# Performance work log

Measured on AMD Instinct MI355X. Metric: run time of the kernel, lower is better.

## Reference

```python
import jax, jax.numpy as jnp
import numpy as np

N_FLUID, N_BOX, K_MAX, KS, NCELL = 6000, 3000, 80, 4, 64
RADIUS = np.float32(0.5 * 1.5 * 6 * 0.025)  # filter_extent / 2 = 0.1125


def _ball_to_cube(p):
    """Volume-preserving ball->cube mapping (open3d ContinuousConv convention).
    p: [..., 3] coordinates in the unit ball; returns coords in [-1,1]^3."""
    eps = 1e-12
    x, y, z = p[..., 0], p[..., 1], p[..., 2]
    sq = x * x + y * y + z * z
    norm = jnp.sqrt(sq)
    rxy2 = x * x + y * y
    # sphere -> cylinder (volume preserving)
    polar = 1.25 * z * z > rxy2
    s_pol = jnp.sqrt(3.0 * norm / (norm + jnp.abs(z) + eps))
    s_eq = norm / jnp.sqrt(rxy2 + eps)
    xc = jnp.where(polar, s_pol * x, s_eq * x)
    yc = jnp.where(polar, s_pol * y, s_eq * y)
    zc = jnp.where(polar, jnp.sign(z) * norm, 1.5 * z * s_eq)
    zero = sq < 1e-12
    xc = jnp.where(zero, 0.0, xc)
    yc = jnp.where(zero, 0.0, yc)
    zc = jnp.where(zero, 0.0, zc)
    # cylinder -> cube (area-preserving disc -> square on xy)
    rxy = jnp.sqrt(xc * xc + yc * yc)
    FP = 4.0 / np.pi
    safe_x = jnp.where(jnp.abs(xc) < eps, eps, xc)
    safe_y = jnp.where(jnp.abs(yc) < eps, eps, yc)
    cond = jnp.abs(xc) >= jnp.abs(yc)
    u1 = jnp.sign(xc) * rxy
    v1 = u1 * FP * jnp.arctan(yc / safe_x)
    v2 = jnp.sign(yc) * rxy
    u2 = v2 * FP * jnp.arctan(xc / safe_y)
    u = jnp.where(cond, u1, u2)
    v = jnp.where(cond, v1, v2)
    small = rxy < eps
    u = jnp.where(small, 0.0, u)
    v = jnp.where(small, 0.0, v)
    return jnp.stack([u, v, zc], axis=-1)


def build_neighbors(pos_in, pos_out, ignore_self):
    """Fixed-radius neighbor search (capped at K_MAX) + window + trilinear
    interpolation cells/weights. Returns idx [No,K], cells [No,K,8] int32,
    coef [No,K,8] (trilinear weight * poly6 window * validity)."""
    d = pos_in[None, :, :] - pos_out[:, None, :]            # [No,Ni,3]
    d2 = jnp.sum(d * d, axis=-1)
    if ignore_self:
        ii = jnp.arange(pos_out.shape[0])
        d2 = jnp.where(ii[:, None] == ii[None, :], jnp.inf, d2)
    neg = jnp.where(d2 <= RADIUS * RADIUS, -d2, -jnp.inf)
    vals, idx = jax.lax.top_k(neg, K_MAX)                   # [No,K]
    valid = (vals > -jnp.inf).astype(pos_in.dtype)
    rel = (pos_in[idx] - pos_out[:, None, :]) / RADIUS      # [No,K,3] unit ball
    r2 = jnp.sum(rel * rel, axis=-1)
    win = jnp.clip((1.0 - r2) ** 3, 0.0, 1.0) * valid       # poly6 window
    g = jnp.clip((_ball_to_cube(rel) + 1.0) * 0.5 * (KS - 1), 0.0, KS - 1.0)
    i0 = jnp.clip(jnp.floor(g), 0, KS - 2).astype(jnp.int32)
    t = g - i0.astype(g.dtype)
    cells, tw = [], []
    for dx in (0, 1):
        for dy in (0, 1):
            for dz in (0, 1):
                w = ((t[..., 0] if dx else 1.0 - t[..., 0])
                     * (t[..., 1] if dy else 1.0 - t[..., 1])
                     * (t[..., 2] if dz else 1.0 - t[..., 2]))
                cell = ((i0[..., 2] + dz) * KS + (i0[..., 1] + dy)) * KS + (i0[..., 0] + dx)
                cells.append(cell)
                tw.append(w)
    cells = jnp.stack(cells, axis=-1)                       # [No,K,8]
    coef = jnp.stack(tw, axis=-1) * win[..., None]          # [No,K,8]
    return idx, cells, coef


def apply_cconv(feats_in, idx, cells, coef, W, b):
    """Continuous conv: scatter neighbor feats into 64 kernel cells per query,
    then contract with the filter. W: [64, F, O]."""
    N, K = idx.shape
    F = feats_in.shape[-1]
    nf = feats_in[idx]                                      # [N,K,F]
    S = jnp.zeros((N * NCELL, F), feats_in.dtype)
    row = (jnp.arange(N, dtype=jnp.int32) * NCELL)[:, None]
    for c in range(8):                                      # 8 trilinear corners
        flat = (row + cells[..., c]).reshape(-1)
        S = S.at[flat].add((coef[..., c:c + 1] * nf).reshape(-1, F))
    return jnp.einsum('ncf,cfo->no', S.reshape(N, NCELL, F), W) + b


def setup_inputs() -> dict:
    key = jax.random.key(0)
    ks = jax.random.split(key, 16)

    def p(i, shape, scale=0.05):
        return (scale * jax.random.normal(ks[i], shape)).astype(jnp.float32)

    return {
        'pos': jax.random.uniform(ks[0], (N_FLUID, 3), dtype=jnp.float32),
        'vel': jax.random.normal(ks[1], (N_FLUID, 3), dtype=jnp.float32),
        'box': jax.random.uniform(ks[2], (N_BOX, 3), dtype=jnp.float32),
        'box_feats': jax.random.normal(ks[3], (N_BOX, 3), dtype=jnp.float32),
        'cf_w': p(4, (NCELL, 4, 32)), 'cf_b': jnp.zeros((32,), jnp.float32),
        'co_w': p(5, (NCELL, 3, 32)), 'co_b': jnp.zeros((32,), jnp.float32),
        'd0_w': p(6, (4, 32)), 'd0_b': jnp.zeros((32,), jnp.float32),
        'c1_w': p(7, (NCELL, 96, 64)), 'c1_b': jnp.zeros((64,), jnp.float32),
        'd1_w': p(8, (96, 64)), 'd1_b': jnp.zeros((64,), jnp.float32),
        'c2_w': p(9, (NCELL, 64, 64)), 'c2_b': jnp.zeros((64,), jnp.float32),
        'd2_w': p(10, (64, 64)), 'd2_b': jnp.zeros((64,), jnp.float32),
        'c3_w': p(11, (NCELL, 64, 3)), 'c3_b': jnp.zeros((3,), jnp.float32),
        'd3_w': p(12, (64, 3)), 'd3_b': jnp.zeros((3,), jnp.float32),
    }


def reference(pos, vel, box, box_feats, cf_w, cf_b, co_w, co_b, d0_w, d0_b,
              c1_w, c1_b, d1_w, d1_b, c2_w, c2_b, d2_w, d2_b, c3_w, c3_b,
              d3_w, d3_b):
    fidx, fcells, fcoef = build_neighbors(pos, pos, True)
    oidx, ocells, ocoef = build_neighbors(box, pos, False)
    ff = jnp.concatenate([jnp.ones_like(pos[:, :1]), vel], axis=-1)  # [N,4]
    a_cf = apply_cconv(ff, fidx, fcells, fcoef, cf_w, cf_b)
    a_co = apply_cconv(box_feats, oidx, ocells, ocoef, co_w, co_b)
    a_d0 = ff @ d0_w + d0_b
    x = jnp.concatenate([a_co, a_cf, a_d0], axis=-1)                 # [N,96]
    for cw, cb, dw, db in ((c1_w, c1_b, d1_w, d1_b),
                           (c2_w, c2_b, d2_w, d2_b),
                           (c3_w, c3_b, d3_w, d3_b)):
        h = jax.nn.relu(x)
        y = apply_cconv(h, fidx, fcells, fcoef, cw, cb) + (h @ dw + db)
        x = y + x if y.shape[-1] == x.shape[-1] else y
    return x * (1.0 / 128.0)  # pos_correction [N,3]
```

## Files before the change

### kernel.cpp

```cpp
#include <hip/hip_runtime.h>
#include <math.h>

namespace {

constexpr int NQ  = 6000;
constexpr int NB  = 3000;
constexpr int K   = 80;
constexpr float RAD = 0.1125f;
constexpr float R2  = RAD * RAD;
constexpr float EPSF = 1e-12f;

constexpr int GS  = 8;
constexpr int NC  = GS*GS*GS;
constexpr int NO  = 65 * 64;
constexpr int NBLK = (NQ + 3) / 4;
constexpr int NBLK8 = ((NBLK + 7) / 8) * 8;

typedef __attribute__((ext_vector_type(8))) short bf16x8;
typedef __attribute__((ext_vector_type(4))) float f32x4;

__device__ __forceinline__ float sgn(float x) {
    return (x > 0.f) ? 1.f : ((x < 0.f) ? -1.f : 0.f);
}

__device__ __forceinline__ unsigned int bf16rne(float f) {
    unsigned int u = __float_as_uint(f);
    return (u + 0x7fffu + ((u >> 16) & 1u)) >> 16;
}
__device__ __forceinline__ float bf16f(unsigned short u) {
    return __uint_as_float(((unsigned int)u) << 16);
}
__device__ __forceinline__ int cell_of(float x, float y, float z) {
    int cx = min(max((int)(x * (float)GS), 0), GS-1);
    int cy = min(max((int)(y * (float)GS), 0), GS-1);
    int cz = min(max((int)(z * (float)GS), 0), GS-1);
    return (cz*GS + cy)*GS + cx;
}

__device__ void coef_store(float ddx, float ddy, float ddz, int slot,
                           int* __restrict__ cells, float* __restrict__ coefs)
{
    float rx = ddx / RAD, ry = ddy / RAD, rz = ddz / RAD;
    float r2 = rx*rx + ry*ry + rz*rz;
    float w1 = 1.f - r2;
    float win = (w1 > 0.f) ? w1*w1*w1 : 0.f;
    float norm = sqrtf(r2);
    float rxy2 = rx*rx + ry*ry;
    float xc, yc, zc;
    if (r2 < 1e-12f) {
        xc = yc = zc = 0.f;
    } else if (1.25f * rz * rz > rxy2) {
        float s = sqrtf(3.0f * norm / (norm + fabsf(rz) + EPSF));
        xc = s * rx; yc = s * ry; zc = sgn(rz) * norm;
    } else {
        float s = norm / sqrtf(rxy2 + EPSF);
        xc = s * rx; yc = s * ry; zc = 1.5f * rz * s;
    }
    float rxy = sqrtf(xc*xc + yc*yc);
    const float FP = (float)(4.0 / M_PI);
    float u, v;
    if (rxy < EPSF) {
        u = 0.f; v = 0.f;
    } else if (fabsf(xc) >= fabsf(yc)) {
        float sx = (fabsf(xc) < EPSF) ? EPSF : xc;
        u = sgn(xc) * rxy;
        v = u * FP * atanf(yc / sx);
    } else {
        float sy = (fabsf(yc) < EPSF) ? EPSF : yc;
        v = sgn(yc) * rxy;
        u = v * FP * atanf(xc / sy);
    }
    float gx = fminf(fmaxf((u  + 1.f) * 0.5f * 3.f, 0.f), 3.f);
    float gy = fminf(fmaxf((v  + 1.f) * 0.5f * 3.f, 0.f), 3.f);
    float gz = fminf(fmaxf((zc + 1.f) * 0.5f * 3.f, 0.f), 3.f);
    int ix = min((int)floorf(gx), 2);
    int iy = min((int)floorf(gy), 2);
    int iz = min((int)floorf(gz), 2);
    float tx = gx - (float)ix, ty = gy - (float)iy, tz = gz - (float)iz;
    cells[slot] = iz*16 + iy*4 + ix;
    float wx[2] = {1.f - tx, tx}, wy[2] = {1.f - ty, ty}, wz[2] = {1.f - tz, tz};
    float* cf = coefs + (size_t)slot * 8;
#pragma unroll
    for (int c = 0; c < 8; ++c)
        cf[c] = wx[c >> 2] * wy[(c >> 1) & 1] * wz[c & 1] * win;
}

__global__ __launch_bounds__(512) void scan_kernel(
    const int* __restrict__ gcnt,
    int* __restrict__ gs_f, int* __restrict__ gs_b,
    int* __restrict__ cur_f, int* __restrict__ cur_b)
{
    __shared__ int tmp[NC];
    int tid = threadIdx.x;
#pragma unroll
    for (int a = 0; a < 2; ++a) {
        int cntv = gcnt[a*NC + tid];
        tmp[tid] = cntv;
        __syncthreads();
        for (int off = 1; off < NC; off <<= 1) {
            int v = (tid >= off) ? tmp[tid - off] : 0;
            __syncthreads();
            tmp[tid] += v;
            __syncthreads();
        }
        int* gsd = a ? gs_b : gs_f;
        int* cur = a ? cur_b : cur_f;
        int excl = tmp[tid] - cntv;
        gsd[tid] = excl;
        cur[tid] = excl;
        if (tid == NC - 1) gsd[NC] = tmp[tid];
        __syncthreads();
    }
}

__global__ __launch_bounds__(256) void scatter_pts_kernel(
    const float* __restrict__ pos, const float* __restrict__ box,
    int* __restrict__ cur_f, int* __restrict__ cur_b,
    float* __restrict__ spf, int* __restrict__ sif,
    float* __restrict__ spb, int* __restrict__ sib)
{
    int t = blockIdx.x * blockDim.x + threadIdx.x;
    if (t < NQ) {
        float x = pos[t*3], y = pos[t*3+1], z = pos[t*3+2];
        int dst = atomicAdd(&cur_f[cell_of(x,y,z)], 1);
        spf[dst*3] = x; spf[dst*3+1] = y; spf[dst*3+2] = z;
        sif[dst] = t;
    } else if (t < NQ + NB) {
        int b = t - NQ;
        float x = box[b*3], y = box[b*3+1], z = box[b*3+2];
        int dst = atomicAdd(&cur_b[cell_of(x,y,z)], 1);
        spb[dst*3] = x; spb[dst*3+1] = y; spb[dst*3+2] = z;
        sib[dst] = b;
    }
}

__global__ __launch_bounds__(256) void nn2gc_kernel(
    const float* __restrict__ pos,
    const float* __restrict__ spf, const int* __restrict__ sif, const int* __restrict__ gsf,
    const float* __restrict__ spb, const int* __restrict__ sib, const int* __restrict__ gsb,
    int* __restrict__ f_cnt, int* __restrict__ f_idx, float* __restrict__ f_d2,
    int* __restrict__ f_cell, float* __restrict__ f_coef,
    int* __restrict__ b_cnt, int* __restrict__ b_idx, float* __restrict__ b_d2,
    int* __restrict__ b_cell, float* __restrict__ b_coef)
{
    int gw = (blockIdx.x * blockDim.x + threadIdx.x) >> 6;
    int lane = threadIdx.x & 63;
    if (gw >= 2 * NQ) return;
    bool isF = gw < NQ;
    int wid = isF ? gw : gw - NQ;
    const float* sp = isF ? spf : spb;
    const int*   si = isF ? sif : sib;
    const int*   gs = isF ? gsf : gsb;
    int*   cnt   = isF ? f_cnt  : b_cnt;
    int*   idxs  = isF ? f_idx  : b_idx;
    float* d2s   = isF ? f_d2   : b_d2;
    int*   cells = isF ? f_cell : b_cell;
    float* coefs = isF ? f_coef : b_coef;
    float qx = pos[wid*3+0], qy = pos[wid*3+1], qz = pos[wid*3+2];
    int cx = min(max((int)(qx * (float)GS), 0), GS-1);
    int cy = min(max((int)(qy * (float)GS), 0), GS-1);
    int cz = min(max((int)(qz * (float)GS), 0), GS-1);
    int x0 = max(cx-1, 0), x1 = min(cx+1, GS-1);
    int base = wid * K;
    int c = 0;
    for (int dz = -1; dz <= 1; ++dz) {
        int z = cz + dz; if ((unsigned)z >= (unsigned)GS) continue;
        for (int dy = -1; dy <= 1; ++dy) {
            int y = cy + dy; if ((unsigned)y >= (unsigned)GS) continue;
            int row = (z*GS + y)*GS;
            int s0 = gs[row + x0], s1 = gs[row + x1 + 1];
            for (int j0 = s0; j0 < s1; j0 += 64) {
                int ii = j0 + lane;
                float d2 = 1e30f; int oj = 0;
                float ddx = 0.f, ddy = 0.f, ddz = 0.f;
                if (ii < s1) {
                    oj = si[ii];
                    ddx = sp[ii*3+0]-qx; ddy = sp[ii*3+1]-qy; ddz = sp[ii*3+2]-qz;
                    d2 = ddx*ddx + ddy*ddy + ddz*ddz;
                    if (isF && oj == wid) d2 = 1e30f;
                }
                bool hit = d2 <= R2;
                unsigned long long m = __ballot(hit);
                int pc = __popcll(m);
                if (pc == 0) continue;
                if (c + pc <= K) {
                    if (hit) {
                        int p = c + __popcll(m & ((1ull << lane) - 1ull));
                        idxs[base + p] = oj;
                        d2s [base + p] = d2;
                        coef_store(ddx, ddy, ddz, base + p, cells, coefs);
                    }
                    c += pc;
                } else {
                    while (m) {
                        int l = __ffsll((unsigned long long)m) - 1;
                        m &= m - 1ull;
                        float dd = __shfl(d2, l);
                        int jv = __shfl(oj, l);
                        float ax = __shfl(ddx, l), ay = __shfl(ddy, l), az = __shfl(ddz, l);
                        int slot = -1;
                        if (c < K) { slot = c; c++; }
                        else {
                            float mx = -1.f; int am = 0;
                            for (int s = 0; s < K; ++s) {
                                float v = d2s[base + s];
                                if (v > mx) { mx = v; am = s; }
                            }
                            if (dd < mx) slot = am;
                        }
                        if (slot >= 0 && lane == 0) {
                            idxs[base + slot] = jv;
                            d2s [base + slot] = dd;
                            coef_store(ax, ay, az, base + slot, cells, coefs);
                        }
                    }
                }
            }
        }
    }
    if (lane == 0) cnt[wid] = c;
}

template<int F>
__device__ void scatter_small_dev(
    const float* __restrict__ feats,
    const int* __restrict__ cnt, const int* __restrict__ nidx,
    const int* __restrict__ ncell, const float* __restrict__ ncoef,
    float* __restrict__ Sg, int blk)
{
    __shared__ __align__(16) float S4[4][64 * F];
    int tid = threadIdx.x, lane = tid & 63, w = tid >> 6;
    int n = blk * 4 + w;
    if (n >= NQ) return;
    float* Sw = S4[w];
    for (int i = lane; i < 64 * F; i += 64) Sw[i] = 0.f;
    int cn = cnt[n];
    int kk2 = 64 + lane;
    int cb1 = (lane < cn) ? ncell[n*K + lane] : 0;
    int j1  = (lane < cn) ? nidx [n*K + lane] : 0;
    int cb2 = (kk2 < cn) ? ncell[n*K + kk2] : 0;
    int j2  = (kk2 < cn) ? nidx [n*K + kk2] : 0;
    int c = lane & 7, f = lane >> 3;
    bool fok = f < F;
    const float* coefG = ncoef + (size_t)n * K * 8;

    float wgt = 0.f, v = 0.f; int cb = 0;
    if (cn > 0) {
        int j = __shfl(j1, 0); cb = __shfl(cb1, 0);
        if (fok) { wgt = coefG[c]; v = feats[(size_t)j * F + f]; }
    }
    for (int kk = 0; kk < cn; ++kk) {
        float wn = 0.f, vn = 0.f; int cbn = 0;
        int k1n = kk + 1;
        if (k1n < cn) {
            int jn = (k1n < 64) ? __shfl(j1, k1n) : __shfl(j2, k1n - 64);
            cbn    = (k1n < 64) ? __shfl(cb1, k1n) : __shfl(cb2, k1n - 64);
            if (fok) { wn = coefG[k1n*8 + c]; vn = feats[(size_t)jn * F + f]; }
        }
        if (fok) {
            int cell = cb + (c & 1)*16 + ((c >> 1) & 1)*4 + (c >> 2);
            Sw[cell*F + f] += wgt * v;
        }
        wgt = wn; v = vn; cb = cbn;
    }
    float* row = Sg + (size_t)n * (64 * F);
    for (int i = lane; i < 16 * F; i += 64)
        ((float4*)row)[i] = ((const float4*)Sw)[i];
}

__global__ __launch_bounds__(256) void scatter0_kernel(
    const float* __restrict__ ff,
    const int* __restrict__ f_cnt, const int* __restrict__ f_idx,
    const int* __restrict__ f_cell, const float* __restrict__ f_coef,
    const float* __restrict__ bfeat,
    const int* __restrict__ b_cnt, const int* __restrict__ b_idx,
    const int* __restrict__ b_cell, const float* __restrict__ b_coef,
    float* __restrict__ S_cf, float* __restrict__ S_co)
{
    constexpr int FB = (NQ + 3) / 4;
    if (blockIdx.x < FB)
        scatter_small_dev<4>(ff, f_cnt, f_idx, f_cell, f_coef, S_cf, blockIdx.x);
    else
        scatter_small_dev<3>(bfeat, b_cnt, b_idx, b_cell, b_coef, S_co, blockIdx.x - FB);
}

__global__ __launch_bounds__(256) void gemm0_kernel(
    const float* __restrict__ S_co, const float* __restrict__ S_cf,
    const float* __restrict__ coW, const float* __restrict__ cfW,
    const float* __restrict__ cob, const float* __restrict__ cfb,
    float* __restrict__ x1, int M)
{
    constexpr int O = 32, TX = 8, MT = 128, ASTR = 132;
    __shared__ float As[16][ASTR];
    __shared__ float Bs[16 * O];
    int which = blockIdx.y;
    const float* A    = which ? S_cf : S_co;
    const float* B    = which ? cfW  : coW;
    const float* bias = which ? cfb  : cob;
    int Kdim = which ? 256 : 192;
    int ooff = which ? 32 : 0;
    int tid = threadIdx.x;
    int tx = tid % TX, ty = tid / TX;
    int m0 = blockIdx.x * MT;
    int ntiles = Kdim >> 4;
    float acc[4][4] = {};
    for (int t = 0; t < ntiles; ++t) {
        int k0 = t << 4;
        __syncthreads();
#pragma unroll
        for (int l = 0; l < 2; ++l) {
            int idx = tid + l * 256;
            int mm = idx >> 2, k4 = idx & 3;
            int gm = m0 + mm; if (gm >= M) gm = M - 1;
            float4 av = *reinterpret_cast<const float4*>(A + (size_t)gm * Kdim + k0 + k4 * 4);
            As[k4*4+0][mm] = av.x; As[k4*4+1][mm] = av.y;
            As[k4*4+2][mm] = av.z; As[k4*4+3][mm] = av.w;
        }
        if (tid < 128)
            *reinterpret_cast<float4*>(&Bs[tid*4]) =
                *reinterpret_cast<const float4*>(B + (size_t)k0 * O + tid * 4);
        __syncthreads();
#pragma unroll
        for (int kk = 0; kk < 16; ++kk) {
            float4 av = *reinterpret_cast<const float4*>(&As[kk][ty*4]);
            float4 bv = *reinterpret_cast<const float4*>(&Bs[kk*O + tx*4]);
            float aa[4] = {av.x, av.y, av.z, av.w};
            float bb[4] = {bv.x, bv.y, bv.z, bv.w};
#pragma unroll
            for (int i = 0; i < 4; ++i)
#pragma unroll
                for (int jj = 0; jj < 4; ++jj)
                    acc[i][jj] += aa[i] * bb[jj];
        }
    }
#pragma unroll
    for (int i = 0; i < 4; ++i) {
        int gm = m0 + ty*4 + i;
        if (gm < M)
#pragma unroll
            for (int jj = 0; jj < 4; ++jj)
                x1[(size_t)gm * 96 + ooff + tx*4 + jj] = acc[i][jj] + bias[tx*4 + jj];
    }
}

template<int F>
__global__ __launch_bounds__(256) void gemmGm_kernel(
    const float* __restrict__ feats,
    const unsigned short* __restrict__ Bt,
    unsigned short* __restrict__ G,
    int M)
{
    constexpr int AST = F + 8;
    __shared__ unsigned short As[64 * AST];
    __shared__ unsigned short Bs[64 * AST];
    int tid = threadIdx.x, lane = tid & 63, wv = tid >> 6;
    int m0 = blockIdx.x * 64, no0 = blockIdx.y * 64;
    for (int i = tid; i < 64 * F / 4; i += 256) {
        int m = i / (F / 4), k4 = i % (F / 4);
        int gm = m0 + m; if (gm >= M) gm = M - 1;
        float4 av = *reinterpret_cast<const float4*>(feats + (size_t)gm * F + k4 * 4);
        uint2 o;
        o.x = bf16rne(fmaxf(av.x, 0.f)) | (bf16rne(fmaxf(av.y, 0.f)) << 16);
        o.y = bf16rne(fmaxf(av.z, 0.f)) | (bf16rne(fmaxf(av.w, 0.f)) << 16);
        *reinterpret_cast<uint2*>(As + m * AST + k4 * 4) = o;
    }
    for (int i = tid; i < 64 * F / 8; i += 256) {
        int n = i / (F / 8), k8 = i % (F / 8);
        *reinterpret_cast<uint4*>(Bs + n * AST + k8 * 8) =
            *reinterpret_cast<const uint4*>(Bt + (size_t)(no0 + n) * F + k8 * 8);
    }
    __syncthreads();
    int mr = lane & 15, quad = lane >> 4;
    f32x4 acc[4] = {{0.f,0.f,0.f,0.f},{0.f,0.f,0.f,0.f},
                    {0.f,0.f,0.f,0.f},{0.f,0.f,0.f,0.f}};
#pragma unroll
    for (int kc = 0; kc < F; kc += 32) {
        bf16x8 a = *reinterpret_cast<const bf16x8*>(As + (wv*16 + mr) * AST + kc + quad*8);
#pragma unroll
        for (int t = 0; t < 4; ++t) {
            bf16x8 b = *reinterpret_cast<const bf16x8*>(Bs + (t*16 + mr) * AST + kc + quad*8);
            acc[t] = __builtin_amdgcn_mfma_f32_16x16x32_bf16(a, b, acc[t], 0, 0, 0);
        }
    }
#pragma unroll
    for (int t = 0; t < 4; ++t) {
#pragma unroll
        for (int r = 0; r < 4; ++r) {
            int gm = m0 + wv*16 + quad*4 + r;
            if (gm < M)
                G[(size_t)gm * NO + no0 + t*16 + mr] = (unsigned short)bf16rne(acc[t][r]);
        }
    }
}

template<int FUSEY>
__global__ __launch_bounds__(256) void gatherG_kernel(
    const int* __restrict__ order,
    const int* __restrict__ cnt, const int* __restrict__ nidx,
    const int* __restrict__ ncell, const float* __restrict__ ncoef,
    const unsigned short* __restrict__ G,
    const float* __restrict__ cb, const float* __restrict__ db,
    const float* __restrict__ resid, float* __restrict__ out,
    const float* __restrict__ W3p, float* __restrict__ Y)
{
    __shared__ __align__(16) float coefL[4][K * 8];
    __shared__ float xs[4][64];
    __shared__ int qn[4];
    int lb = (blockIdx.x & 7) * (gridDim.x >> 3) + (blockIdx.x >> 3);
    int tid = threadIdx.x;
    int wv = tid >> 6, lane = tid & 63;
    int w = lb * 4 + wv;
    bool valid = w < NQ;
    if (!FUSEY && !valid) return;
    int n = valid ? order[w] : 0;
    int cn = valid ? cnt[n] : 0;
    {
        const float4* src = (const float4*)(ncoef + (size_t)n * K * 8);
        float4* dst = (float4*)coefL[wv];
        for (int i = lane; i < cn * 2; i += 64) dst[i] = src[i];
    }
    int kk2 = 64 + lane;
    int cb1 = (lane < cn) ? ncell[n*K + lane] : 0;
    int j1  = (lane < cn) ? nidx [n*K + lane] : 0;
    int cb2 = (kk2 < cn) ? ncell[n*K + kk2] : 0;
    int j2  = (kk2 < cn) ? nidx [n*K + kk2] : 0;
    float a0 = 0.f, a1 = 0.f, a2 = 0.f, a3 = 0.f;
    const float* cwv = coefL[wv];
    int c1e = min(cn, 64);
#pragma unroll 4
    for (int k = 0; k < c1e; ++k) {
        int j    = __shfl(j1, k);
        int cbse = __shfl(cb1, k);
        float4 cA = *reinterpret_cast<const float4*>(cwv + k*8);
        float4 cB = *reinterpret_cast<const float4*>(cwv + k*8 + 4);
        const unsigned short* Gj = G + (size_t)j * NO + lane;
        a0 += cA.x * bf16f(Gj[(cbse     ) * 64]);
        a1 += cA.y * bf16f(Gj[(cbse + 16) * 64]);
        a2 += cA.z * bf16f(Gj[(cbse +  4) * 64]);
        a3 += cA.w * bf16f(Gj[(cbse + 20) * 64]);
        a0 += cB.x * bf16f(Gj[(cbse +  1) * 64]);
        a1 += cB.y * bf16f(Gj[(cbse + 17) * 64]);
        a2 += cB.z * bf16f(Gj[(cbse +  5) * 64]);
        a3 += cB.w * bf16f(Gj[(cbse + 21) * 64]);
    }
    for (int k = 64; k < cn; ++k) {
        int j    = __shfl(j2, k - 64);
        int cbse = __shfl(cb2, k - 64);
        float4 cA = *reinterpret_cast<const float4*>(cwv + k*8);
        float4 cB = *reinterpret_cast<const float4*>(cwv + k*8 + 4);
        const unsigned short* Gj = G + (size_t)j * NO + lane;
        a0 += cA.x * bf16f(Gj[(cbse     ) * 64]);
        a1 += cA.y * bf16f(Gj[(cbse + 16) * 64]);
        a2 += cA.z * bf16f(Gj[(cbse +  4) * 64]);
        a3 += cA.w * bf16f(Gj[(cbse + 20) * 64]);
        a0 += cB.x * bf16f(Gj[(cbse +  1) * 64]);
        a1 += cB.y * bf16f(Gj[(cbse + 17) * 64]);
        a2 += cB.z * bf16f(Gj[(cbse +  5) * 64]);
        a3 += cB.w * bf16f(Gj[(cbse + 21) * 64]);
    }
    float acc = cb[lane] + db[lane] + ((a0 + a1) + (a2 + a3));
    acc += bf16f(G[(size_t)n * NO + 64*64 + lane]);
    if (resid) acc += resid[(size_t)n * 64 + lane];
    if (!FUSEY) {
        out[(size_t)n * 64 + lane] = acc;
    } else {
        xs[wv][lane] = valid ? fmaxf(acc, 0.f) : 0.f;
        if (lane == 0) qn[wv] = valid ? n : -1;
        __syncthreads();
        for (int idx = tid; idx < 4 * 195; idx += 256) {
            int q = idx / 195, t = idx - q * 195;
            int nn = qn[q];
            if (nn >= 0) {
                float s = 0.f;
#pragma unroll 16
                for (int f = 0; f < 64; ++f) s += xs[q][f] * W3p[f*195 + t];
                Y[(size_t)nn * 195 + t] = s;
            }
        }
    }
}

__global__ __launch_bounds__(256) void prep_kernel(
    const float* __restrict__ c1w, const float* __restrict__ d1w,
    const float* __restrict__ c2w, const float* __restrict__ d2w,
    const float* __restrict__ c3w, const float* __restrict__ d3w,
    const float* __restrict__ pos, const float* __restrict__ box,
    const float* __restrict__ vel,
    const float* __restrict__ d0w, const float* __restrict__ d0b,
    unsigned short* __restrict__ Bt1, unsigned short* __restrict__ Bt2,
    float* __restrict__ W3p, float* __restrict__ ff, float* __restrict__ x1,
    int* __restrict__ gcnt)
{
    int stride = gridDim.x * blockDim.x;
    int gid = blockIdx.x * blockDim.x + threadIdx.x;
    for (int i = gid; i < NQ + NB; i += stride) {
        const float* p = (i < NQ) ? pos + (size_t)i*3 : box + (size_t)(i-NQ)*3;
        atomicAdd(&gcnt[((i < NQ) ? 0 : NC) + cell_of(p[0], p[1], p[2])], 1);
    }
    for (int i = gid; i < NO * 96; i += stride) {
        int n = i / 96, f = i % 96, c = n >> 6, o = n & 63;
        float v = (c < 64) ? c1w[((size_t)c*96 + f)*64 + o] : d1w[f*64 + o];
        Bt1[i] = (unsigned short)bf16rne(v);
    }
    for (int i = gid; i < NO * 64; i += stride) {
        int n = i / 64, f = i % 64, c = n >> 6, o = n & 63;
        float v = (c < 64) ? c2w[((size_t)c*64 + f)*64 + o] : d2w[f*64 + o];
        Bt2[i] = (unsigned short)bf16rne(v);
    }
    for (int i = gid; i < 64 * 195; i += stride) {
        int f = i / 195, r = i % 195, c = r / 3, o = r % 3;
        W3p[i] = (c < 64) ? c3w[(c*64 + f)*3 + o] : d3w[f*3 + o];
    }
    for (int i = gid; i < NQ; i += stride) {
        ff[i*4+0] = 1.f;
        ff[i*4+1] = vel[i*3+0];
        ff[i*4+2] = vel[i*3+1];
        ff[i*4+3] = vel[i*3+2];
    }
    for (int i = gid; i < NQ * 32; i += stride) {
        int n = i >> 5, o = i & 31;
        float acc = d0b[o] + d0w[o]
                  + vel[n*3+0] * d0w[32 + o]
                  + vel[n*3+1] * d0w[64 + o]
                  + vel[n*3+2] * d0w[96 + o];
        x1[n*96 + 64 + o] = acc;
    }
}

__global__ __launch_bounds__(256) void gather3_kernel(
    const int* __restrict__ order,
    const int* __restrict__ cnt, const int* __restrict__ nidx,
    const int* __restrict__ ncell, const float* __restrict__ ncoef,
    const float* __restrict__ Y,
    const float* __restrict__ cb3, const float* __restrict__ db3,
    float* __restrict__ out)
{
    int lb = (blockIdx.x & 7) * (gridDim.x >> 3) + (blockIdx.x >> 3);
    int gw = lb * 4 + ((int)threadIdx.x >> 6);
    int lane = threadIdx.x & 63;
    if (gw >= NQ) return;
    int n = order[gw];
    int cn = cnt[n];
    float a0 = 0.f, a1 = 0.f, a2 = 0.f;
#pragma unroll
    for (int seg = 0; seg < 2; ++seg) {
        int kidx = seg * 64 + lane;
        if (kidx < cn) {
            int j  = nidx [n*K + kidx];
            int cb = ncell[n*K + kidx];
            const float* cf = ncoef + (size_t)(n*K + kidx) * 8;
            const float* Yj = Y + (size_t)j * 195;
#pragma unroll
            for (int c = 0; c < 8; ++c) {
                int cell = cb + (c & 1)*16 + ((c >> 1) & 1)*4 + (c >> 2);
                float wgt = cf[c];
                const float* Tp = Yj + cell*3;
                a0 += wgt * Tp[0];
                a1 += wgt * Tp[1];
                a2 += wgt * Tp[2];
            }
        }
    }
#pragma unroll
    for (int s = 32; s > 0; s >>= 1) {
        a0 += __shfl_down(a0, s);
        a1 += __shfl_down(a1, s);
        a2 += __shfl_down(a2, s);
    }
    if (lane == 0) {
        const float* Yn = Y + (size_t)n * 195 + 192;
        out[n*3+0] = (a0 + Yn[0] + cb3[0] + db3[0]) * (1.f/128.f);
        out[n*3+1] = (a1 + Yn[1] + cb3[1] + db3[1]) * (1.f/128.f);
        out[n*3+2] = (a2 + Yn[2] + cb3[2] + db3[2]) * (1.f/128.f);
    }
}

}

extern "C" void kernel_launch(void* const* d_in, const int* in_sizes, int n_in,
                              void* d_out, int out_size, void* d_ws, size_t ws_size,
                              hipStream_t stream)
{
    const float* pos       = (const float*)d_in[0];
    const float* vel       = (const float*)d_in[1];
    const float* box       = (const float*)d_in[2];
    const float* box_feats = (const float*)d_in[3];
    const float* cf_w = (const float*)d_in[4];  const float* cf_b = (const float*)d_in[5];
    const float* co_w = (const float*)d_in[6];  const float* co_b = (const float*)d_in[7];
    const float* d0_w = (const float*)d_in[8];  const float* d0_b = (const float*)d_in[9];
    const float* c1_w = (const float*)d_in[10]; const float* c1_b = (const float*)d_in[11];
    const float* d1_w = (const float*)d_in[12]; const float* d1_b = (const float*)d_in[13];
    const float* c2_w = (const float*)d_in[14]; const float* c2_b = (const float*)d_in[15];
    const float* d2_w = (const float*)d_in[16]; const float* d2_b = (const float*)d_in[17];
    const float* c3_w = (const float*)d_in[18]; const float* c3_b = (const float*)d_in[19];
    const float* d3_w = (const float*)d_in[20]; const float* d3_b = (const float*)d_in[21];

    char* wsb = (char*)d_ws;
    size_t off = 0;
    auto alloc = [&](size_t bytes) {
        void* p = wsb + off;
        off = (off + bytes + 255) & ~(size_t)255;
        return p;
    };
    char*  Graw = (char*)alloc((size_t)NQ * NO * 2 + 4096);
    unsigned short* G = (unsigned short*)Graw;
    float* f_d2 = (float*)Graw;
    float* b_d2 = (float*)Graw + (size_t)NQ * K;
    float* S_cf = (float*)Graw;
    float* S_co = (float*)Graw + (size_t)NQ * 256;
    int*   f_cnt  = (int*)  alloc((size_t)NQ * 4);
    int*   f_idx  = (int*)  alloc((size_t)NQ * K * 4);
    int*   f_cell = (int*)  alloc((size_t)NQ * K * 4);
    float* f_coef = (float*)alloc((size_t)NQ * K * 8 * 4);
    int*   b_cnt  = (int*)  alloc((size_t)NQ * 4);
    int*   b_idx  = (int*)  alloc((size_t)NQ * K * 4);
    int*   b_cell = (int*)  alloc((size_t)NQ * K * 4);
    float* b_coef = (float*)alloc((size_t)NQ * K * 8 * 4);
    float* ff     = (float*)alloc((size_t)NQ * 4 * 4);
    float* x1     = (float*)alloc((size_t)NQ * 96 * 4);
    float* x2     = (float*)alloc((size_t)NQ * 64 * 4);
    unsigned short* Bt1 = (unsigned short*)alloc((size_t)NO * 96 * 2);
    unsigned short* Bt2 = (unsigned short*)alloc((size_t)NO * 64 * 2);
    float* W3p    = (float*)alloc((size_t)64 * 195 * 4);
    float* Y      = (float*)alloc((size_t)NQ * 195 * 4);
    int*   gcnt   = (int*)  alloc((size_t)2 * NC * 4);
    int*   gs_f   = (int*)  alloc((size_t)(NC + 1) * 4);
    int*   gs_b   = (int*)  alloc((size_t)(NC + 1) * 4);
    int*   cur_f  = (int*)  alloc((size_t)NC * 4);
    int*   cur_b  = (int*)  alloc((size_t)NC * 4);
    float* spf    = (float*)alloc((size_t)NQ * 3 * 4);
    int*   sif    = (int*)  alloc((size_t)NQ * 4);
    float* spb    = (float*)alloc((size_t)NB * 3 * 4);
    int*   sib    = (int*)  alloc((size_t)NB * 4);

    dim3 b256(256);
    hipMemsetAsync(gcnt, 0, (size_t)2 * NC * 4, stream);
    prep_kernel<<<512, b256, 0, stream>>>(c1_w, d1_w, c2_w, d2_w, c3_w, d3_w,
                                          pos, box, vel, d0_w, d0_b,
                                          Bt1, Bt2, W3p, ff, x1, gcnt);
    scan_kernel<<<1, 512, 0, stream>>>(gcnt, gs_f, gs_b, cur_f, cur_b);
    scatter_pts_kernel<<<(NQ + NB + 255)/256, b256, 0, stream>>>(
        pos, box, cur_f, cur_b, spf, sif, spb, sib);
    nn2gc_kernel<<<(2*NQ*64 + 255)/256, b256, 0, stream>>>(
        pos, spf, sif, gs_f, spb, sib, gs_b,
        f_cnt, f_idx, f_d2, f_cell, f_coef,
        b_cnt, b_idx, b_d2, b_cell, b_coef);
    scatter0_kernel<<<2*((NQ+3)/4), b256, 0, stream>>>(
        ff, f_cnt, f_idx, f_cell, f_coef,
        box_feats, b_cnt, b_idx, b_cell, b_coef, S_cf, S_co);
    gemm0_kernel<<<dim3((NQ+127)/128, 2), b256, 0, stream>>>(
        S_co, S_cf, co_w, cf_w, co_b, cf_b, x1, NQ);
    gemmGm_kernel<96><<<dim3((NQ+63)/64, NO/64), b256, 0, stream>>>(x1, Bt1, G, NQ);
    gatherG_kernel<0><<<NBLK8, b256, 0, stream>>>(sif, f_cnt, f_idx, f_cell, f_coef,
        G, c1_b, d1_b, nullptr, x2, nullptr, nullptr);
    gemmGm_kernel<64><<<dim3((NQ+63)/64, NO/64), b256, 0, stream>>>(x2, Bt2, G, NQ);
    gatherG_kernel<1><<<NBLK8, b256, 0, stream>>>(sif, f_cnt, f_idx, f_cell, f_coef,
        G, c2_b, d2_b, x2, nullptr, W3p, Y);
    gather3_kernel<<<NBLK8, b256, 0, stream>>>(sif, f_cnt, f_idx, f_cell, f_coef,
        Y, c3_b, d3_b, (float*)d_out);

    (void)in_sizes; (void)n_in; (void)out_size; (void)ws_size;
    (void)f_d2; (void)b_d2;
}
```

Measured before the change: 291.3 us.

## Interleave G columns by cell groups of four for vectorized 8-byte gathers

The weight permutation in prep is changed so the GEMM output G stores four consecutive cells interleaved per output channel. The gather loop can then fetch four bf16 values with one 8-byte load and pick out the needed pair with a shift, using four loads per neighbor instead of eight 2-byte loads. The aim is fewer memory transactions in the gather-bound cconv kernel, at the cost of more bytes fetched per load and some extra shift and mask ALU work.

Result: slower. 312.3 us (+7.2%).

```diff
diff --git a/kernel.cpp b/kernel.cpp
--- a/kernel.cpp
+++ b/kernel.cpp
@@ -15,6 +15,7 @@
 constexpr int NO  = 65 * 64;
 constexpr int NBLK = (NQ + 3) / 4;
 constexpr int NBLK8 = ((NBLK + 7) / 8) * 8;
+
 
 typedef __attribute__((ext_vector_type(8))) short bf16x8;
 typedef __attribute__((ext_vector_type(4))) float f32x4;
@@ -426,6 +427,7 @@
     int j2  = (kk2 < cn) ? nidx [n*K + kk2] : 0;
     float a0 = 0.f, a1 = 0.f, a2 = 0.f, a3 = 0.f;
     const float* cwv = coefL[wv];
+    const uint2* Gw = reinterpret_cast<const uint2*>(G);
     int c1e = min(cn, 64);
 #pragma unroll 4
     for (int k = 0; k < c1e; ++k) {
@@ -433,30 +435,48 @@
         int cbse = __shfl(cb1, k);
         float4 cA = *reinterpret_cast<const float4*>(cwv + k*8);
         float4 cB = *reinterpret_cast<const float4*>(cwv + k*8 + 4);
-        const unsigned short* Gj = G + (size_t)j * NO + lane;
-        a0 += cA.x * bf16f(Gj[(cbse     ) * 64]);
-        a1 += cA.y * bf16f(Gj[(cbse + 16) * 64]);
-        a2 += cA.z * bf16f(Gj[(cbse +  4) * 64]);
-        a3 += cA.w * bf16f(Gj[(cbse + 20) * 64]);
-        a0 += cB.x * bf16f(Gj[(cbse +  1) * 64]);
-        a1 += cB.y * bf16f(Gj[(cbse + 17) * 64]);
-        a2 += cB.z * bf16f(Gj[(cbse +  5) * 64]);
-        a3 += cB.w * bf16f(Gj[(cbse + 21) * 64]);
+        int sh = (cbse & 3) * 16;
+        const uint2* Gj = Gw + (size_t)j * (NO/4) + (cbse >> 2) * 64 + lane;
+        uint2 v00 = Gj[0];
+        uint2 v01 = Gj[64];
+        uint2 v10 = Gj[256];
+        uint2 v11 = Gj[320];
+        unsigned long long d00 = v00.x | ((unsigned long long)v00.y << 32);
+        unsigned long long d01 = v01.x | ((unsigned long long)v01.y << 32);
+        unsigned long long d10 = v10.x | ((unsigned long long)v10.y << 32);
+        unsigned long long d11 = v11.x | ((unsigned long long)v11.y << 32);
+        unsigned int p00 = (unsigned int)(d00 >> sh);
+        unsigned int p01 = (unsigned int)(d01 >> sh);
+        unsigned int p10 = (unsigned int)(d10 >> sh);
+        unsigned int p11 = (unsigned int)(d11 >> sh);
+        a0 += cA.x * __uint_as_float(p00 << 16) + cB.x * __uint_as_float(p00 & 0xffff0000u);
+        a1 += cA.y * __uint_as_float(p10 << 16) + cB.y * __uint_as_float(p10 & 0xffff0000u);
+        a2 += cA.z * __uint_as_float(p01 << 16) + cB.z * __uint_as_float(p01 & 0xffff0000u);
+        a3 += cA.w * __uint_as_float(p11 << 16) + cB.w * __uint_as_float(p11 & 0xffff0000u);
     }
     for (int k = 64; k < cn; ++k) {
         int j    = __shfl(j2, k - 64);
         int cbse = __shfl(cb2, k - 64);
         float4 cA = *reinterpret_cast<const float4*>(cwv + k*8);
         float4 cB = *reinterpret_cast<const float4*>(cwv + k*8 + 4);
-        const unsigned short* Gj = G + (size_t)j * NO + lane;
-        a0 += cA.x * bf16f(Gj[(cbse     ) * 64]);
-        a1 += cA.y * bf16f(Gj[(cbse + 16) * 64]);
-        a2 += cA.z * bf16f(Gj[(cbse +  4) * 64]);
-        a3 += cA.w * bf16f(Gj[(cbse + 20) * 64]);
-        a0 += cB.x * bf16f(Gj[(cbse +  1) * 64]);
-        a1 += cB.y * bf16f(Gj[(cbse + 17) * 64]);
-        a2 += cB.z * bf16f(Gj[(cbse +  5) * 64]);
-        a3 += cB.w * bf16f(Gj[(cbse + 21) * 64]);
+        int sh = (cbse & 3) * 16;
+        const uint2* Gj = Gw + (size_t)j * (NO/4) + (cbse >> 2) * 64 + lane;
+        uint2 v00 = Gj[0];
+        uint2 v01 = Gj[64];
+        uint2 v10 = Gj[256];
+        uint2 v11 = Gj[320];
+        unsigned long long d00 = v00.x | ((unsigned long long)v00.y << 32);
+        unsigned long long d01 = v01.x | ((unsigned long long)v01.y << 32);
+        unsigned long long d10 = v10.x | ((unsigned long long)v10.y << 32);
+        unsigned long long d11 = v11.x | ((unsigned long long)v11.y << 32);
+        unsigned int p00 = (unsigned int)(d00 >> sh);
+        unsigned int p01 = (unsigned int)(d01 >> sh);
+        unsigned int p10 = (unsigned int)(d10 >> sh);
+        unsigned int p11 = (unsigned int)(d11 >> sh);
+        a0 += cA.x * __uint_as_float(p00 << 16) + cB.x * __uint_as_float(p00 & 0xffff0000u);
+        a1 += cA.y * __uint_as_float(p10 << 16) + cB.y * __uint_as_float(p10 & 0xffff0000u);
+        a2 += cA.z * __uint_as_float(p01 << 16) + cB.z * __uint_as_float(p01 & 0xffff0000u);
+        a3 += cA.w * __uint_as_float(p11 << 16) + cB.w * __uint_as_float(p11 & 0xffff0000u);
     }
     float acc = cb[lane] + db[lane] + ((a0 + a1) + (a2 + a3));
     acc += bf16f(G[(size_t)n * NO + 64*64 + lane]);
@@ -498,12 +518,18 @@
         atomicAdd(&gcnt[((i < NQ) ? 0 : NC) + cell_of(p[0], p[1], p[2])], 1);
     }
     for (int i = gid; i < NO * 96; i += stride) {
-        int n = i / 96, f = i % 96, c = n >> 6, o = n & 63;
+        int np = i / 96, f = i % 96;
+        int c, o;
+        if (np >= 4096) { c = 64; o = np - 4096; }
+        else { int cg = np >> 8, rem = np & 255; o = rem >> 2; c = cg*4 + (rem & 3); }
         float v = (c < 64) ? c1w[((size_t)c*96 + f)*64 + o] : d1w[f*64 + o];
         Bt1[i] = (unsigned short)bf16rne(v);
     }
     for (int i = gid; i < NO * 64; i += stride) {
-        int n = i / 64, f = i % 64, c = n >> 6, o = n & 63;
+        int np = i / 64, f = i % 64;
+        int c, o;
+        if (np >= 4096) { c = 64; o = np - 4096; }
+        else { int cg = np >> 8, rem = np & 255; o = rem >> 2; c = cg*4 + (rem & 3); }
         float v = (c < 64) ? c2w[((size_t)c*64 + f)*64 + o] : d2w[f*64 + o];
         Bt2[i] = (unsigned short)bf16rne(v);
     }
```
